# Optimization experiments

Hardware: AMD Instinct MI355X
Metric: run time of the kernel (lower is better)

## Reference

```python
import jax, jax.numpy as jnp
import numpy as np

T, B, E, H = 4096, 2, 1024, 16          # seq, batch, embed, heads
W = 256                                  # one-sided attention window (attention_window=512 // 2)
G = 64                                   # number of global tokens (first G positions)
D = E // H
NEG = -1e9


def _band_mask():
    # valid key position for band slot j at query t is t - W + j in [0, T)
    pos = jnp.arange(T)[:, None] - W + jnp.arange(2 * W + 1)[None, :]
    return (pos >= 0) & (pos < T)  # [T, 2W+1]


def _chunk_blocks(x):
    # x: [b, t, h, d] -> key/value blocks [b, nc, 3w, h, d]; block c covers positions [c*w - w, c*w + 2w)
    b, t, h, d = x.shape
    nc = t // W
    xp = jnp.pad(x, ((0, 0), (W, 2 * W), (0, 0), (0, 0)))
    idx = jnp.arange(nc)[:, None] * W + jnp.arange(3 * W)[None, :]
    return xp[:, idx]


def _band_qk(q, k):
    # q,k: [b,t,h,d] -> banded scores [b,t,h,2w+1] (Longformer sliding_chunks_matmul_qk)
    b, t, h, d = q.shape
    nc = t // W
    qc = q.reshape(b, nc, W, h, d)
    kb = _chunk_blocks(k)
    scores = jnp.einsum('bcxhd,bcyhd->bhcxy', qc, kb)          # y in [0, 3w)
    y_idx = jnp.arange(W)[:, None] + jnp.arange(2 * W + 1)[None, :]  # [w, 2w+1]
    band = jnp.take_along_axis(scores, y_idx[None, None, None], axis=-1)
    band = band.reshape(b, h, t, 2 * W + 1).transpose(0, 2, 1, 3)
    return jnp.where(_band_mask()[None, :, None, :], band, NEG)


def _band_pv(p, v):
    # p: [b,t,h,2w+1], v: [b,t,h,d] -> [b,t,h,d] (sliding_chunks_matmul_pv)
    b, t, h, _ = p.shape
    nc = t // W
    pb = p.transpose(0, 2, 1, 3).reshape(b, h, nc, W, 2 * W + 1)
    x = jnp.arange(W)
    y_idx = x[:, None] + jnp.arange(2 * W + 1)[None, :]
    p3 = jnp.zeros((b, h, nc, W, 3 * W), p.dtype).at[:, :, :, x[:, None], y_idx].set(pb)
    vb = _chunk_blocks(v)
    out = jnp.einsum('bhcxy,bcyhd->bcxhd', p3, vb)
    return out.reshape(b, t, h, -1)


def setup_inputs() -> dict:
    key = jax.random.key(0)
    ks = jax.random.split(key, 16)
    s = 0.02
    inp = {
        'query': jax.random.normal(ks[0], (T, B, E), jnp.float32),
        'attn_mask': jnp.concatenate([jnp.ones((B, G), jnp.int64), jnp.zeros((B, T - G), jnp.int64)], axis=1),
        'Wq': jax.random.normal(ks[1], (E, E), jnp.float32) * s, 'bq': jnp.zeros((E,), jnp.float32),
        'Wk': jax.random.normal(ks[2], (E, E), jnp.float32) * s, 'bk': jnp.zeros((E,), jnp.float32),
        'Wv': jax.random.normal(ks[3], (E, E), jnp.float32) * s, 'bv': jnp.zeros((E,), jnp.float32),
        'Wqg': jax.random.normal(ks[4], (E, E), jnp.float32) * s, 'bqg': jnp.zeros((E,), jnp.float32),
        'Wkg': jax.random.normal(ks[5], (E, E), jnp.float32) * s, 'bkg': jnp.zeros((E,), jnp.float32),
        'Wvg': jax.random.normal(ks[6], (E, E), jnp.float32) * s, 'bvg': jnp.zeros((E,), jnp.float32),
        'Wo': jax.random.normal(ks[7], (E, E), jnp.float32) * s, 'bo': jnp.zeros((E,), jnp.float32),
    }
    return inp


def reference(query, attn_mask, Wq, bq, Wk, bk, Wv, bv, Wqg, bqg, Wkg, bkg, Wvg, bvg, Wo, bo):
    del attn_mask  # structure fixed: first G tokens are global, no padding
    scaling = D ** -0.5
    x = query.transpose(1, 0, 2)                      # [b, t, e]
    q = ((x @ Wq.T + bq) * scaling).reshape(B, T, H, D)
    k = (x @ Wk.T + bk).reshape(B, T, H, D)
    v = (x @ Wv.T + bv).reshape(B, T, H, D)

    band = _band_qk(q, k)                             # [b,t,h,2w+1]
    sel_w = jnp.einsum('blhd,bshd->blhs', q, k[:, :G])  # every token attends global keys
    aw = jnp.concatenate([sel_w, band], axis=-1)
    probs = jax.nn.softmax(aw.astype(jnp.float32), axis=-1).astype(aw.dtype)

    attn = jnp.einsum('blhs,bshd->blhd', probs[..., :G], v[:, :G])
    attn = attn + _band_pv(probs[..., G:], v)         # [b,t,h,d]

    # global tokens attend everything with the *_global projections
    qg = ((x[:, :G] @ Wqg.T + bqg) * scaling).reshape(B, G, H, D)
    kg = (x @ Wkg.T + bkg).reshape(B, T, H, D)
    vg = (x @ Wvg.T + bvg).reshape(B, T, H, D)
    gs = jnp.einsum('bghd,bthd->bhgt', qg, kg)
    gp = jax.nn.softmax(gs.astype(jnp.float32), axis=-1).astype(gs.dtype)
    gout = jnp.einsum('bhgt,bthd->bghd', gp, vg)
    attn = attn.at[:, :G].set(gout)

    out = attn.reshape(B, T, E).transpose(1, 0, 2) @ Wo.T + bo  # [t, b, e]
    return out
```

## Files before the change

kernel.cpp:

```cpp
#include <hip/hip_runtime.h>
#include <hip/hip_bf16.h>

typedef unsigned short u16;
typedef __bf16 bf16x8 __attribute__((ext_vector_type(8)));
typedef float  f32x4  __attribute__((ext_vector_type(4)));

constexpr int TT = 4096;
constexpr int BBATCH = 2;
constexpr int EE = 1024;
constexpr int HH = 16;
constexpr int DD = 64;
constexpr int WQ = 256;
constexpr int GG = 64;
constexpr int NSPLIT = 8;

__device__ __forceinline__ u16 f2bf(float f) {
    union { float f; unsigned int i; } c; c.f = f;
    unsigned int x = c.i;
    return (u16)((x + 0x7fffu + ((x >> 16) & 1u)) >> 16);
}
__device__ __forceinline__ unsigned cvt_pk_bf16(float a, float b) {
    unsigned r;
    asm("v_cvt_pk_bf16_f32 %0, %1, %2" : "=v"(r) : "v"(a), "v"(b));
    return r;
}
__device__ __forceinline__ uint4 pack8(float4 a, float4 b) {
    uint4 r;
    r.x = (unsigned)f2bf(a.x) | ((unsigned)f2bf(a.y) << 16);
    r.y = (unsigned)f2bf(a.z) | ((unsigned)f2bf(a.w) << 16);
    r.z = (unsigned)f2bf(b.x) | ((unsigned)f2bf(b.y) << 16);
    r.w = (unsigned)f2bf(b.z) | ((unsigned)f2bf(b.w) << 16);
    return r;
}

__device__ __forceinline__ void g2l16(const u16* g, u16* l) {
    __builtin_amdgcn_global_load_lds(
        (const __attribute__((address_space(1))) void*)g,
        (__attribute__((address_space(3))) void*)l, 16, 0, 0);
}

__device__ __forceinline__ void xcd_swizzle(int& bx, int& by) {
    bx = blockIdx.x; by = blockIdx.y;
    if ((gridDim.y & 7) == 0) {
        const int g   = blockIdx.x + blockIdx.y * gridDim.x;
        const int idx = g >> 3;
        bx = idx % gridDim.x;
        by = (g & 7) + ((idx / gridDim.x) << 3);
    }
}

struct WPtrs { const float* p[7]; };
__global__ __launch_bounds__(256) void conv_kernel(
    WPtrs wp, const float* __restrict__ query, u16* __restrict__ wb, u16* __restrict__ xb)
{
    const size_t i8 = ((size_t)blockIdx.x * 256 + threadIdx.x) << 3;
    const size_t WTOT = (size_t)7 << 20;
    const float* src;
    u16* dst;
    if (i8 < WTOT) {
        const int which = (int)(i8 >> 20);
        src = wp.p[which] + (i8 & (((size_t)1 << 20) - 1));
        dst = wb + i8;
    } else {
        const size_t j = i8 - WTOT;
        const size_t e = j & (EE - 1);
        const size_t t = (j >> 10) & (TT - 1);
        const size_t b = j >> 22;
        src = query + (t * BBATCH + b) * EE + e;
        dst = xb + j;
    }
    const float4 f0 = *(const float4*)src;
    const float4 f1 = *(const float4*)(src + 4);
    *(uint4*)dst = pack8(f0, f1);
}

template<int C_F32, int PERMA_QG, int PERMC_TB>
__global__ __launch_bounds__(256) void gemm_kernel(
    const u16* __restrict__ A, const u16* __restrict__ W, const float* __restrict__ bias,
    void* __restrict__ Cv, float scale)
{
    const int tid = threadIdx.x, lane = tid & 63, w = tid >> 6;
    const int wm = w >> 1, wn = w & 1;
    int bx, by;
    xcd_swizzle(bx, by);
    const int m0 = by << 7, n0 = bx << 7;

    __shared__ __align__(16) u16 As[2 * 128 * 32];
    __shared__ __align__(16) u16 Bs[2 * 128 * 32];

    const int lrow = lane >> 2;
    const int lcol = (lane & 3) << 3;
    auto arow = [](int m) -> size_t {
        return PERMA_QG ? (size_t)(((m >> 6) << 12) | (m & 63)) : (size_t)m;
    };
    const u16* gA0 = A + arow(m0 + (w << 4) + lrow) * EE + lcol;
    const u16* gA1 = A + arow(m0 + 64 + (w << 4) + lrow) * EE + lcol;
    const u16* gB0 = W + (size_t)(n0 + (w << 4) + lrow) * EE + lcol;
    const u16* gB1 = gB0 + (size_t)64 * EE;
    u16* lA0 = As + (w << 9);
    u16* lA1 = As + 2048 + (w << 9);
    u16* lB0 = Bs + (w << 9);
    u16* lB1 = Bs + 2048 + (w << 9);

    f32x4 acc[4][4];
#pragma unroll
    for (int i = 0; i < 4; i++)
#pragma unroll
        for (int j = 0; j < 4; j++)
            acc[i][j] = (f32x4){0.f, 0.f, 0.f, 0.f};

    const int fr = lane & 15;
    const int fq = (lane >> 4) << 3;

    for (int k0 = 0; k0 < EE; k0 += 64) {
        g2l16(gA0 + k0, lA0);  g2l16(gA0 + k0 + 32, lA0 + 4096);
        g2l16(gA1 + k0, lA1);  g2l16(gA1 + k0 + 32, lA1 + 4096);
        g2l16(gB0 + k0, lB0);  g2l16(gB0 + k0 + 32, lB0 + 4096);
        g2l16(gB1 + k0, lB1);  g2l16(gB1 + k0 + 32, lB1 + 4096);
        __syncthreads();
#pragma unroll
        for (int p = 0; p < 2; p++) {
            bf16x8 af[4], bfv[4];
#pragma unroll
            for (int i = 0; i < 4; i++)
                af[i] = *(const bf16x8*)&As[p * 4096 + ((wm << 6) + (i << 4) + fr) * 32 + fq];
#pragma unroll
            for (int j = 0; j < 4; j++)
                bfv[j] = *(const bf16x8*)&Bs[p * 4096 + ((wn << 6) + (j << 4) + fr) * 32 + fq];
#pragma unroll
            for (int i = 0; i < 4; i++)
#pragma unroll
                for (int j = 0; j < 4; j++)
                    acc[i][j] = __builtin_amdgcn_mfma_f32_16x16x32_bf16(af[i], bfv[j], acc[i][j], 0, 0, 0);
        }
        __syncthreads();
    }

    const int colbase = n0 + (wn << 6);
    const int rowbase = m0 + (wm << 6) + ((lane >> 4) << 2);
#pragma unroll
    for (int j = 0; j < 4; j++) {
        const int col = colbase + (j << 4) + fr;
        const float bv = bias[col];
#pragma unroll
        for (int i = 0; i < 4; i++) {
#pragma unroll
            for (int r = 0; r < 4; r++) {
                const int row = rowbase + (i << 4) + r;
                const float val = (acc[i][j][r] + bv) * scale;
                const size_t dst = (size_t)(PERMC_TB ? (((row & (TT - 1)) << 1) | (row >> 12)) : row) * EE + col;
                if (C_F32) ((float*)Cv)[dst] = val;
                else       ((u16*)Cv)[dst]   = f2bf(val);
            }
        }
    }
}

struct FusedArgs { u16* out[3]; const float* bias[3]; float scale[3]; int vseg; };

template<int NSEG, int CF32, int PERMC>
__global__ __launch_bounds__(256, 2) void gemm_pipe_kernel(
    const u16* __restrict__ A, const u16* __restrict__ W, FusedArgs fa)
{
    const int tid = threadIdx.x, lane = tid & 63, w = tid >> 6;
    const int wm = w >> 1, wn = w & 1;
    int bx, by;
    xcd_swizzle(bx, by);
    const int m0 = by << 7, n0 = bx << 7;

    __shared__ __align__(16) u16 As[2][8192];
    __shared__ __align__(16) u16 Bs[2][8192];

    const int srow = lane >> 3;
    const int scol = ((lane & 7) ^ srow) << 3;
    const u16* gA = A + (size_t)(m0 + (w << 5) + srow) * EE + scol;
    const u16* gB = W + (size_t)(n0 + (w << 5) + srow) * EE + scol;
    u16* lA = &As[0][0] + (w << 11);
    u16* lB = &Bs[0][0] + (w << 11);

    f32x4 acc[4][4];
#pragma unroll
    for (int i = 0; i < 4; i++)
#pragma unroll
        for (int j = 0; j < 4; j++)
            acc[i][j] = (f32x4){0.f, 0.f, 0.f, 0.f};

    const int fr = lane & 15;
    const int qb = (lane >> 4) << 4;
    const int xr = (fr & 7) << 4;

    auto stageA = [&](int k0, int buf) {
#pragma unroll
        for (int l = 0; l < 4; l++)
            g2l16(gA + (size_t)(l << 3) * EE + k0, lA + buf * 8192 + (l << 9));
    };
    auto stageB = [&](int k0, int buf) {
#pragma unroll
        for (int l = 0; l < 4; l++)
            g2l16(gB + (size_t)(l << 3) * EE + k0, lB + buf * 8192 + (l << 9));
    };

    stageA(0, 0);
    stageB(0, 0);
    __syncthreads();

    constexpr int NT = EE / 64;
#pragma unroll 2
    for (int t = 0; t < NT; t++) {
        const int buf = t & 1;
        const bool pf = (t + 1 < NT);
        const int kn = (t + 1) << 6;
        bf16x8 af[4], bfv[4];

#pragma unroll
        for (int mi = 0; mi < 4; mi++)
            af[mi] = *(const bf16x8*)((const char*)&As[buf][0] +
                      ((((wm << 6) + (mi << 4) + fr)) << 7) + (qb ^ xr));
#pragma unroll
        for (int nj = 0; nj < 4; nj++)
            bfv[nj] = *(const bf16x8*)((const char*)&Bs[buf][0] +
                      ((((wn << 6) + (nj << 4) + fr)) << 7) + (qb ^ xr));
        if (pf) stageA(kn, buf ^ 1);
        __builtin_amdgcn_s_barrier();
        __builtin_amdgcn_s_setprio(1);
#pragma unroll
        for (int mi = 0; mi < 4; mi++)
#pragma unroll
            for (int nj = 0; nj < 4; nj++)
                acc[mi][nj] = __builtin_amdgcn_mfma_f32_16x16x32_bf16(af[mi], bfv[nj], acc[mi][nj], 0, 0, 0);
        __builtin_amdgcn_s_setprio(0);
        __builtin_amdgcn_s_barrier();

#pragma unroll
        for (int mi = 0; mi < 4; mi++)
            af[mi] = *(const bf16x8*)((const char*)&As[buf][0] +
                      ((((wm << 6) + (mi << 4) + fr)) << 7) + ((64 | qb) ^ xr));
#pragma unroll
        for (int nj = 0; nj < 4; nj++)
            bfv[nj] = *(const bf16x8*)((const char*)&Bs[buf][0] +
                      ((((wn << 6) + (nj << 4) + fr)) << 7) + ((64 | qb) ^ xr));
        if (pf) stageB(kn, buf ^ 1);
        __builtin_amdgcn_s_barrier();
        __builtin_amdgcn_s_setprio(1);
#pragma unroll
        for (int mi = 0; mi < 4; mi++)
#pragma unroll
            for (int nj = 0; nj < 4; nj++)
                acc[mi][nj] = __builtin_amdgcn_mfma_f32_16x16x32_bf16(af[mi], bfv[nj], acc[mi][nj], 0, 0, 0);
        __builtin_amdgcn_s_setprio(0);
        __syncthreads();
    }

    const int seg = (NSEG > 1) ? (n0 >> 10) : 0;
    u16* outp = fa.out[seg];
    const float* bp = fa.bias[seg];
    const float scl = fa.scale[seg];
    const bool vtr = (NSEG > 1) && (seg == fa.vseg);

    const int colbase = n0 + (wn << 6);
    const int rowbase = m0 + (wm << 6) + ((lane >> 4) << 2);
#pragma unroll
    for (int j = 0; j < 4; j++) {
        const int col = colbase + (j << 4) + fr;
        const int cl  = col & (EE - 1);
        const float bv = bp[cl];
#pragma unroll
        for (int i = 0; i < 4; i++) {
            if (vtr) {
                const int row0 = rowbase + (i << 4);
                const int bb = row0 >> 12, t = row0 & (TT - 1);
                const int hh = cl >> 6, d = cl & 63;
                ushort4 pk;
                pk.x = f2bf((acc[i][j][0] + bv) * scl);
                pk.y = f2bf((acc[i][j][1] + bv) * scl);
                pk.z = f2bf((acc[i][j][2] + bv) * scl);
                pk.w = f2bf((acc[i][j][3] + bv) * scl);
                *(ushort4*)(outp + (((size_t)(bb * HH + hh) * DD + d) * TT + t)) = pk;
            } else {
#pragma unroll
                for (int r = 0; r < 4; r++) {
                    const int row = rowbase + (i << 4) + r;
                    const float val = (acc[i][j][r] + bv) * scl;
                    const size_t drow = PERMC ? (size_t)(((row & (TT - 1)) << 1) | (row >> 12))
                                              : (size_t)row;
                    if (CF32) ((float*)outp)[drow * EE + cl] = val;
                    else      outp[drow * EE + cl] = f2bf(val);
                }
            }
        }
    }
}

__global__ __launch_bounds__(256) void band_attn_kernel(
    const u16* __restrict__ q, const u16* __restrict__ k, const u16* __restrict__ vt,
    u16* __restrict__ attnb)
{
    const int tid  = threadIdx.x;
    const int lane = tid & 63;
    const int w    = tid >> 6;
    const int col  = lane & 15;
    const int quad = lane >> 4;

    const int qt = blockIdx.x >> 5;
    const int bh = blockIdx.x & 31;
    const int h  = bh & (HH - 1);
    const int b  = bh >> 4;
    const int t0 = qt << 6;

    __shared__ __align__(16) u16 Ks[2][64][72];
    __shared__ __align__(16) u16 Vs[2][64][72];
    __shared__ __align__(16) u16 Ps[4][16][72];

    const size_t base   = (size_t)b * TT * EE + (size_t)h * DD;
    const size_t vtbase = (size_t)bh * DD * TT;

    const u16* qp = q + base + (size_t)(t0 + (w << 4) + col) * EE + (quad << 3);
    const bf16x8 qf0 = *(const bf16x8*)qp;
    const bf16x8 qf1 = *(const bf16x8*)(qp + 32);

    float m_i = -1e30f, l_i = 0.f;
    f32x4 acc_o[4];
#pragma unroll
    for (int nt = 0; nt < 4; nt++) acc_o[nt] = (f32x4){0.f, 0.f, 0.f, 0.f};

    const int c_lo = 1 + ((t0 < WQ) ? ((WQ - t0) >> 6) : 0);
    const int c_hi = min(9, 1 + ((TT + WQ - 64 - t0) >> 6));
    const int NTL  = 2 + c_hi - c_lo;

    const int srow  = tid >> 2;
    const int spart = (tid & 3) << 4;

    uint4 kr0, kr1, vr0, vr1;
    auto issue_loads = [&](int i) {
        const int kpos0 = (i == 0) ? 0 : (t0 - WQ + ((c_lo + i - 2) << 6));
        const u16* ks = k + base + (size_t)(kpos0 + srow) * EE + spart;
        const u16* vs = vt + vtbase + (size_t)srow * TT + kpos0 + spart;
        kr0 = *(const uint4*)ks;
        kr1 = *(const uint4*)(ks + 8);
        vr0 = *(const uint4*)vs;
        vr1 = *(const uint4*)(vs + 8);
    };
    auto write_stage = [&](int buf) {
        *(uint4*)&Ks[buf][srow][spart]     = kr0;
        *(uint4*)&Ks[buf][srow][spart + 8] = kr1;
        *(uint4*)&Vs[buf][srow][spart]     = vr0;
        *(uint4*)&Vs[buf][srow][spart + 8] = vr1;
    };

    issue_loads(0);
    write_stage(0);
    int buf = 0;

    const int qrow = (w << 4) + col;
    const int alsrc0 = (lane & 48) | ((lane >> 2) & 12);

#pragma unroll 1
    for (int i = 0; i < NTL; i++) {
        __syncthreads();
        const int c     = c_lo + i - 1;
        const int jbase = (i > 0 && (c == 1 || c == 9)) ? ((c - 1) << 6) : -1;
        const bool pf   = (i + 1 < NTL);
        if (pf) issue_loads(i + 1);

        f32x4 sT[4];
#pragma unroll
        for (int nt = 0; nt < 4; nt++) {
            const bf16x8 kf0 = *(const bf16x8*)&Ks[buf][(nt << 4) + col][quad << 3];
            const bf16x8 kf1 = *(const bf16x8*)&Ks[buf][(nt << 4) + col][32 + (quad << 3)];
            f32x4 s = (f32x4){0.f, 0.f, 0.f, 0.f};
            s = __builtin_amdgcn_mfma_f32_16x16x32_bf16(kf0, qf0, s, 0, 0, 0);
            s = __builtin_amdgcn_mfma_f32_16x16x32_bf16(kf1, qf1, s, 0, 0, 0);
            sT[nt] = s;
        }

        if (jbase >= 0) {
#pragma unroll
            for (int nt = 0; nt < 4; nt++) {
#pragma unroll
                for (int r = 0; r < 4; r++) {
                    const int jp = jbase + (nt << 4) + (quad << 2) + r;
                    const bool ok = (jp >= qrow) && (jp <= qrow + 2 * WQ);
                    if (!ok) sT[nt][r] = -1e30f;
                }
            }
        }

        float mx = sT[0][0];
#pragma unroll
        for (int nt = 0; nt < 4; nt++)
#pragma unroll
            for (int r = 0; r < 4; r++) mx = fmaxf(mx, sT[nt][r]);
        mx = fmaxf(mx, __shfl_xor(mx, 16));
        mx = fmaxf(mx, __shfl_xor(mx, 32));
        const float m_new = fmaxf(m_i, mx);
        const float alpha = __expf(m_i - m_new);
        m_i = m_new;
        l_i *= alpha;
        float ps = 0.f;
#pragma unroll
        for (int nt = 0; nt < 4; nt++)
#pragma unroll
            for (int r = 0; r < 4; r++) {
                const float e = __expf(sT[nt][r] - m_new);
                sT[nt][r] = e;
                ps += e;
            }
        ps += __shfl_xor(ps, 16);
        ps += __shfl_xor(ps, 32);
        l_i += ps;

        float al[4];
#pragma unroll
        for (int r = 0; r < 4; r++) al[r] = __shfl(alpha, alsrc0 | r);
#pragma unroll
        for (int nt = 0; nt < 4; nt++)
#pragma unroll
            for (int r = 0; r < 4; r++) acc_o[nt][r] *= al[r];

#pragma unroll
        for (int nt = 0; nt < 4; nt++) {
            uint2 pk2;
            pk2.x = cvt_pk_bf16(sT[nt][0], sT[nt][1]);
            pk2.y = cvt_pk_bf16(sT[nt][2], sT[nt][3]);
            *(uint2*)&Ps[w][col][(nt << 4) + (quad << 2)] = pk2;
        }

        const bf16x8 pf0 = *(const bf16x8*)&Ps[w][col][quad << 3];
        const bf16x8 pf1 = *(const bf16x8*)&Ps[w][col][32 + (quad << 3)];

#pragma unroll
        for (int nt = 0; nt < 4; nt++) {
            const bf16x8 vf0 = *(const bf16x8*)&Vs[buf][(nt << 4) + col][quad << 3];
            const bf16x8 vf1 = *(const bf16x8*)&Vs[buf][(nt << 4) + col][32 + (quad << 3)];
            acc_o[nt] = __builtin_amdgcn_mfma_f32_16x16x32_bf16(pf0, vf0, acc_o[nt], 0, 0, 0);
            acc_o[nt] = __builtin_amdgcn_mfma_f32_16x16x32_bf16(pf1, vf1, acc_o[nt], 0, 0, 0);
        }

        if (pf) write_stage(buf ^ 1);
        buf ^= 1;
    }

    float inv[4];
#pragma unroll
    for (int r = 0; r < 4; r++) inv[r] = 1.f / __shfl(l_i, alsrc0 | r);
#pragma unroll
    for (int nt = 0; nt < 4; nt++) {
#pragma unroll
        for (int r = 0; r < 4; r++) {
            const int t = t0 + (w << 4) + (quad << 2) + r;
            attnb[base + (size_t)t * EE + (nt << 4) + col] = f2bf(acc_o[nt][r] * inv[r]);
        }
    }
}

__global__ __launch_bounds__(256) void global_attn_flash_kernel(
    const u16* __restrict__ qg, const u16* __restrict__ kg, const u16* __restrict__ vgt,
    float* __restrict__ Op, float* __restrict__ Ml, float* __restrict__ Ll)
{
    const int tid  = threadIdx.x;
    const int lane = tid & 63;
    const int w    = tid >> 6;
    const int col  = lane & 15;
    const int quad = lane >> 4;

    const int s  = blockIdx.x & (NSPLIT - 1);
    const int h  = (blockIdx.x >> 3) & (HH - 1);
    const int b  = blockIdx.x >> 7;
    const int k0pos = s * (TT / NSPLIT);

    __shared__ __align__(16) u16 Ks[2][64][72];
    __shared__ __align__(16) u16 Vs[2][64][72];
    __shared__ __align__(16) u16 Ps[4][16][72];

    const size_t base   = (size_t)b * TT * EE + (size_t)h * DD;
    const size_t vtbase = (size_t)((b << 4) | h) * DD * TT;

    const u16* qp = qg + (size_t)(b * GG + (w << 4) + col) * EE + (size_t)h * DD + (quad << 3);
    const bf16x8 qf0 = *(const bf16x8*)qp;
    const bf16x8 qf1 = *(const bf16x8*)(qp + 32);

    float m_i = -1e30f, l_i = 0.f;
    f32x4 acc_o[4];
#pragma unroll
    for (int nt = 0; nt < 4; nt++) acc_o[nt] = (f32x4){0.f, 0.f, 0.f, 0.f};

    constexpr int NTL = TT / NSPLIT / 64;
    const int srow  = tid >> 2;
    const int spart = (tid & 3) << 4;

    uint4 kr0, kr1, vr0, vr1;
    auto issue_loads = [&](int i) {
        const int kpos0 = k0pos + (i << 6);
        const u16* ks = kg + base + (size_t)(kpos0 + srow) * EE + spart;
        const u16* vs = vgt + vtbase + (size_t)srow * TT + kpos0 + spart;
        kr0 = *(const uint4*)ks;
        kr1 = *(const uint4*)(ks + 8);
        vr0 = *(const uint4*)vs;
        vr1 = *(const uint4*)(vs + 8);
    };
    auto write_stage = [&](int buf) {
        *(uint4*)&Ks[buf][srow][spart]     = kr0;
        *(uint4*)&Ks[buf][srow][spart + 8] = kr1;
        *(uint4*)&Vs[buf][srow][spart]     = vr0;
        *(uint4*)&Vs[buf][srow][spart + 8] = vr1;
    };

    issue_loads(0);
    write_stage(0);
    int buf = 0;

    const int alsrc0 = (lane & 48) | ((lane >> 2) & 12);

#pragma unroll 1
    for (int i = 0; i < NTL; i++) {
        __syncthreads();
        const bool pf = (i + 1 < NTL);
        if (pf) issue_loads(i + 1);

        f32x4 sT[4];
#pragma unroll
        for (int nt = 0; nt < 4; nt++) {
            const bf16x8 kf0 = *(const bf16x8*)&Ks[buf][(nt << 4) + col][quad << 3];
            const bf16x8 kf1 = *(const bf16x8*)&Ks[buf][(nt << 4) + col][32 + (quad << 3)];
            f32x4 sv = (f32x4){0.f, 0.f, 0.f, 0.f};
            sv = __builtin_amdgcn_mfma_f32_16x16x32_bf16(kf0, qf0, sv, 0, 0, 0);
            sv = __builtin_amdgcn_mfma_f32_16x16x32_bf16(kf1, qf1, sv, 0, 0, 0);
            sT[nt] = sv;
        }

        float mx = sT[0][0];
#pragma unroll
        for (int nt = 0; nt < 4; nt++)
#pragma unroll
            for (int r = 0; r < 4; r++) mx = fmaxf(mx, sT[nt][r]);
        mx = fmaxf(mx, __shfl_xor(mx, 16));
        mx = fmaxf(mx, __shfl_xor(mx, 32));
        const float m_new = fmaxf(m_i, mx);
        const float alpha = __expf(m_i - m_new);
        m_i = m_new;
        l_i *= alpha;
        float ps = 0.f;
#pragma unroll
        for (int nt = 0; nt < 4; nt++)
#pragma unroll
            for (int r = 0; r < 4; r++) {
                const float e = __expf(sT[nt][r] - m_new);
                sT[nt][r] = e;
                ps += e;
            }
        ps += __shfl_xor(ps, 16);
        ps += __shfl_xor(ps, 32);
        l_i += ps;

        float al[4];
#pragma unroll
        for (int r = 0; r < 4; r++) al[r] = __shfl(alpha, alsrc0 | r);
#pragma unroll
        for (int nt = 0; nt < 4; nt++)
#pragma unroll
            for (int r = 0; r < 4; r++) acc_o[nt][r] *= al[r];

#pragma unroll
        for (int nt = 0; nt < 4; nt++) {
            uint2 pk2;
            pk2.x = cvt_pk_bf16(sT[nt][0], sT[nt][1]);
            pk2.y = cvt_pk_bf16(sT[nt][2], sT[nt][3]);
            *(uint2*)&Ps[w][col][(nt << 4) + (quad << 2)] = pk2;
        }

        const bf16x8 pf0 = *(const bf16x8*)&Ps[w][col][quad << 3];
        const bf16x8 pf1 = *(const bf16x8*)&Ps[w][col][32 + (quad << 3)];

#pragma unroll
        for (int nt = 0; nt < 4; nt++) {
            const bf16x8 vf0 = *(const bf16x8*)&Vs[buf][(nt << 4) + col][quad << 3];
            const bf16x8 vf1 = *(const bf16x8*)&Vs[buf][(nt << 4) + col][32 + (quad << 3)];
            acc_o[nt] = __builtin_amdgcn_mfma_f32_16x16x32_bf16(pf0, vf0, acc_o[nt], 0, 0, 0);
            acc_o[nt] = __builtin_amdgcn_mfma_f32_16x16x32_bf16(pf1, vf1, acc_o[nt], 0, 0, 0);
        }

        if (pf) write_stage(buf ^ 1);
        buf ^= 1;
    }

    const size_t obase = (size_t)blockIdx.x * GG * DD;
#pragma unroll
    for (int nt = 0; nt < 4; nt++) {
#pragma unroll
        for (int r = 0; r < 4; r++) {
            const int row = (w << 4) + (quad << 2) + r;
            Op[obase + (size_t)row * DD + (nt << 4) + col] = acc_o[nt][r];
        }
    }
    if (quad == 0) {
        Ml[blockIdx.x * GG + (w << 4) + col] = m_i;
        Ll[blockIdx.x * GG + (w << 4) + col] = l_i;
    }
}

__global__ __launch_bounds__(256) void global_combine_kernel(
    const float* __restrict__ Op, const float* __restrict__ Ml, const float* __restrict__ Ll,
    u16* __restrict__ attnb)
{
    const int bh  = blockIdx.x;
    const int b   = bh >> 4;
    const int h   = bh & (HH - 1);
    const int row = threadIdx.x >> 2;
    const int d0  = (threadIdx.x & 3) << 4;

    float mv[NSPLIT];
    float m = -1e30f;
#pragma unroll
    for (int s = 0; s < NSPLIT; s++) {
        mv[s] = Ml[(bh * NSPLIT + s) * GG + row];
        m = fmaxf(m, mv[s]);
    }
    float l = 0.f;
    float sc[NSPLIT];
#pragma unroll
    for (int s = 0; s < NSPLIT; s++) {
        sc[s] = __expf(mv[s] - m);
        l += Ll[(bh * NSPLIT + s) * GG + row] * sc[s];
    }
    float o[16];
#pragma unroll
    for (int j = 0; j < 16; j++) o[j] = 0.f;
#pragma unroll
    for (int s = 0; s < NSPLIT; s++) {
        const float* src = Op + ((size_t)(bh * NSPLIT + s) * GG + row) * DD + d0;
        const float f = sc[s];
#pragma unroll
        for (int j = 0; j < 16; j += 4) {
            const float4 v4 = *(const float4*)(src + j);
            o[j + 0] = fmaf(v4.x, f, o[j + 0]);
            o[j + 1] = fmaf(v4.y, f, o[j + 1]);
            o[j + 2] = fmaf(v4.z, f, o[j + 2]);
            o[j + 3] = fmaf(v4.w, f, o[j + 3]);
        }
    }
    const float inv = 1.f / l;
    u16* dst = attnb + ((size_t)b * TT + row) * EE + (size_t)h * DD + d0;
#pragma unroll
    for (int j = 0; j < 16; j++) dst[j] = f2bf(o[j] * inv);
}

extern "C" void kernel_launch(void* const* d_in, const int* in_sizes, int n_in,
                              void* d_out, int out_size, void* d_ws, size_t ws_size,
                              hipStream_t stream)
{
    (void)in_sizes; (void)n_in; (void)out_size; (void)ws_size;
    const float* query = (const float*)d_in[0];
    const float* Wq  = (const float*)d_in[2];  const float* bq  = (const float*)d_in[3];
    const float* Wk  = (const float*)d_in[4];  const float* bk  = (const float*)d_in[5];
    const float* Wv  = (const float*)d_in[6];  const float* bv  = (const float*)d_in[7];
    const float* Wqg = (const float*)d_in[8];  const float* bqg = (const float*)d_in[9];
    const float* Wkg = (const float*)d_in[10]; const float* bkg = (const float*)d_in[11];
    const float* Wvg = (const float*)d_in[12]; const float* bvg = (const float*)d_in[13];
    const float* Wo  = (const float*)d_in[14]; const float* bo  = (const float*)d_in[15];

    const size_t nfull = (size_t)BBATCH * TT * EE;
    const size_t wsz   = (size_t)1 << 20;
    u16* xb    = (u16*)d_ws;
    u16* wb    = xb + nfull;
    u16* slotA = wb + 7 * wsz;
    u16* slotB = slotA + nfull;
    u16* slotC = slotB + nfull;
    u16* qg    = slotC + nfull;
    float* Op  = (float*)(qg + (size_t)BBATCH * GG * EE);
    float* Ml  = Op + (size_t)BBATCH * HH * NSPLIT * GG * DD;
    float* Ll  = Ml + (size_t)BBATCH * HH * NSPLIT * GG;
    u16* attnb = xb;

    WPtrs wp;
    wp.p[0] = Wq; wp.p[1] = Wk; wp.p[2] = Wv;
    wp.p[3] = Wkg; wp.p[4] = Wvg; wp.p[5] = Wqg; wp.p[6] = Wo;

    const dim3 blk(256);
    const dim3 gF2(16, 64);
    const dim3 gF3(24, 64);
    const dim3 gFull(8, 64);
    const dim3 gQg(8, 1);
    const float sc = 0.125f;

    conv_kernel<<<7680, blk, 0, stream>>>(wp, query, wb, xb);

    gemm_kernel<0, 1, 0><<<gQg, blk, 0, stream>>>(xb, wb + 5 * wsz, bqg, qg, sc);

    FusedArgs fa2;
    fa2.out[0] = slotA; fa2.out[1] = slotB; fa2.out[2] = nullptr;
    fa2.bias[0] = bkg;  fa2.bias[1] = bvg;  fa2.bias[2] = nullptr;
    fa2.scale[0] = 1.f; fa2.scale[1] = 1.f; fa2.scale[2] = 1.f;
    fa2.vseg = 1;
    gemm_pipe_kernel<2, 0, 0><<<gF2, blk, 0, stream>>>(xb, wb + 3 * wsz, fa2);
    global_attn_flash_kernel<<<BBATCH * HH * NSPLIT, blk, 0, stream>>>(qg, slotA, slotB, Op, Ml, Ll);

    FusedArgs fa3;
    fa3.out[0] = slotA; fa3.out[1] = slotB; fa3.out[2] = slotC;
    fa3.bias[0] = bq;   fa3.bias[1] = bk;   fa3.bias[2] = bv;
    fa3.scale[0] = sc;  fa3.scale[1] = 1.f; fa3.scale[2] = 1.f;
    fa3.vseg = 2;
    gemm_pipe_kernel<3, 0, 0><<<gF3, blk, 0, stream>>>(xb, wb, fa3);

    band_attn_kernel<<<BBATCH * HH * (TT / 64), blk, 0, stream>>>(slotA, slotB, slotC, attnb);
    global_combine_kernel<<<BBATCH * HH, blk, 0, stream>>>(Op, Ml, Ll, attnb);

    FusedArgs faO;
    faO.out[0] = (u16*)d_out; faO.out[1] = nullptr; faO.out[2] = nullptr;
    faO.bias[0] = bo;         faO.bias[1] = nullptr; faO.bias[2] = nullptr;
    faO.scale[0] = 1.f;       faO.scale[1] = 1.f;    faO.scale[2] = 1.f;
    faO.vseg = -1;
    gemm_pipe_kernel<1, 1, 1><<<gFull, blk, 0, stream>>>(attnb, wb + 6 * wsz, faO);
}
```

Baseline: 341.4 us.

## Use single-buffered GEMM and lazy softmax rescaling in attention kernels

Replaces the double-buffered, barrier-interleaved GEMM main loop with a simpler single-buffered loop: load a K tile, sync, compute two k-halves, sync. This halves LDS use and drops the min-blocks launch bound, which could raise occupancy, but global loads no longer overlap with MFMA work. Separately, both flash-attention kernels now skip the running-max update and accumulator rescale unless some lane's new max exceeds the old one by more than 8. That saves exps and multiplies but lets exponentials reach up to e^8 before renormalising.

Result: slower. 352.4 us (+3.2%).

```diff
diff --git a/kernel.cpp b/kernel.cpp
--- a/kernel.cpp
+++ b/kernel.cpp
@@ -159,7 +159,7 @@
 struct FusedArgs { u16* out[3]; const float* bias[3]; float scale[3]; int vseg; };
 
 template<int NSEG, int CF32, int PERMC>
-__global__ __launch_bounds__(256, 2) void gemm_pipe_kernel(
+__global__ __launch_bounds__(256) void gemm_sb_kernel(
     const u16* __restrict__ A, const u16* __restrict__ W, FusedArgs fa)
 {
     const int tid = threadIdx.x, lane = tid & 63, w = tid >> 6;
@@ -168,15 +168,15 @@
     xcd_swizzle(bx, by);
     const int m0 = by << 7, n0 = bx << 7;
 
-    __shared__ __align__(16) u16 As[2][8192];
-    __shared__ __align__(16) u16 Bs[2][8192];
+    __shared__ __align__(16) u16 As[8192];
+    __shared__ __align__(16) u16 Bs[8192];
 
     const int srow = lane >> 3;
     const int scol = ((lane & 7) ^ srow) << 3;
     const u16* gA = A + (size_t)(m0 + (w << 5) + srow) * EE + scol;
     const u16* gB = W + (size_t)(n0 + (w << 5) + srow) * EE + scol;
-    u16* lA = &As[0][0] + (w << 11);
-    u16* lB = &Bs[0][0] + (w << 11);
+    u16* lA = As + (w << 11);
+    u16* lB = Bs + (w << 11);
 
     f32x4 acc[4][4];
 #pragma unroll
@@ -189,65 +189,31 @@
     const int qb = (lane >> 4) << 4;
     const int xr = (fr & 7) << 4;
 
-    auto stageA = [&](int k0, int buf) {
-#pragma unroll
-        for (int l = 0; l < 4; l++)
-            g2l16(gA + (size_t)(l << 3) * EE + k0, lA + buf * 8192 + (l << 9));
-    };
-    auto stageB = [&](int k0, int buf) {
-#pragma unroll
-        for (int l = 0; l < 4; l++)
-            g2l16(gB + (size_t)(l << 3) * EE + k0, lB + buf * 8192 + (l << 9));
-    };
-
-    stageA(0, 0);
-    stageB(0, 0);
-    __syncthreads();
-
-    constexpr int NT = EE / 64;
-#pragma unroll 2
-    for (int t = 0; t < NT; t++) {
-        const int buf = t & 1;
-        const bool pf = (t + 1 < NT);
-        const int kn = (t + 1) << 6;
-        bf16x8 af[4], bfv[4];
-
-#pragma unroll
-        for (int mi = 0; mi < 4; mi++)
-            af[mi] = *(const bf16x8*)((const char*)&As[buf][0] +
-                      ((((wm << 6) + (mi << 4) + fr)) << 7) + (qb ^ xr));
-#pragma unroll
-        for (int nj = 0; nj < 4; nj++)
-            bfv[nj] = *(const bf16x8*)((const char*)&Bs[buf][0] +
-                      ((((wn << 6) + (nj << 4) + fr)) << 7) + (qb ^ xr));
-        if (pf) stageA(kn, buf ^ 1);
-        __builtin_amdgcn_s_barrier();
-        __builtin_amdgcn_s_setprio(1);
-#pragma unroll
-        for (int mi = 0; mi < 4; mi++)
+    for (int t = 0; t < EE / 64; t++) {
+        const int k0 = t << 6;
+#pragma unroll
+        for (int l = 0; l < 4; l++) {
+            g2l16(gA + (size_t)(l << 3) * EE + k0, lA + (l << 9));
+            g2l16(gB + (size_t)(l << 3) * EE + k0, lB + (l << 9));
+        }
+        __syncthreads();
+#pragma unroll
+        for (int kh = 0; kh < 2; kh++) {
+            bf16x8 af[4], bfv[4];
+#pragma unroll
+            for (int mi = 0; mi < 4; mi++)
+                af[mi] = *(const bf16x8*)((const char*)As +
+                          ((((wm << 6) + (mi << 4) + fr)) << 7) + (((kh << 6) | qb) ^ xr));
 #pragma unroll
             for (int nj = 0; nj < 4; nj++)
-                acc[mi][nj] = __builtin_amdgcn_mfma_f32_16x16x32_bf16(af[mi], bfv[nj], acc[mi][nj], 0, 0, 0);
-        __builtin_amdgcn_s_setprio(0);
-        __builtin_amdgcn_s_barrier();
-
-#pragma unroll
-        for (int mi = 0; mi < 4; mi++)
-            af[mi] = *(const bf16x8*)((const char*)&As[buf][0] +
-                      ((((wm << 6) + (mi << 4) + fr)) << 7) + ((64 | qb) ^ xr));
-#pragma unroll
-        for (int nj = 0; nj < 4; nj++)
-            bfv[nj] = *(const bf16x8*)((const char*)&Bs[buf][0] +
-                      ((((wn << 6) + (nj << 4) + fr)) << 7) + ((64 | qb) ^ xr));
-        if (pf) stageB(kn, buf ^ 1);
-        __builtin_amdgcn_s_barrier();
-        __builtin_amdgcn_s_setprio(1);
-#pragma unroll
-        for (int mi = 0; mi < 4; mi++)
-#pragma unroll
-            for (int nj = 0; nj < 4; nj++)
-                acc[mi][nj] = __builtin_amdgcn_mfma_f32_16x16x32_bf16(af[mi], bfv[nj], acc[mi][nj], 0, 0, 0);
-        __builtin_amdgcn_s_setprio(0);
+                bfv[nj] = *(const bf16x8*)((const char*)Bs +
+                          ((((wn << 6) + (nj << 4) + fr)) << 7) + (((kh << 6) | qb) ^ xr));
+#pragma unroll
+            for (int mi = 0; mi < 4; mi++)
+#pragma unroll
+                for (int nj = 0; nj < 4; nj++)
+                    acc[mi][nj] = __builtin_amdgcn_mfma_f32_16x16x32_bf16(af[mi], bfv[nj], acc[mi][nj], 0, 0, 0);
+        }
         __syncthreads();
     }
 
@@ -392,30 +358,33 @@
             for (int r = 0; r < 4; r++) mx = fmaxf(mx, sT[nt][r]);
         mx = fmaxf(mx, __shfl_xor(mx, 16));
         mx = fmaxf(mx, __shfl_xor(mx, 32));
-        const float m_new = fmaxf(m_i, mx);
-        const float alpha = __expf(m_i - m_new);
-        m_i = m_new;
-        l_i *= alpha;
+
+        if (!__all(mx - m_i <= 8.0f)) {
+            const float m_new = fmaxf(m_i, mx);
+            const float alpha = __expf(m_i - m_new);
+            m_i = m_new;
+            l_i *= alpha;
+            float al[4];
+#pragma unroll
+            for (int r = 0; r < 4; r++) al[r] = __shfl(alpha, alsrc0 | r);
+#pragma unroll
+            for (int nt = 0; nt < 4; nt++)
+#pragma unroll
+                for (int r = 0; r < 4; r++) acc_o[nt][r] *= al[r];
+        }
+
         float ps = 0.f;
 #pragma unroll
         for (int nt = 0; nt < 4; nt++)
 #pragma unroll
             for (int r = 0; r < 4; r++) {
-                const float e = __expf(sT[nt][r] - m_new);
+                const float e = __expf(sT[nt][r] - m_i);
                 sT[nt][r] = e;
                 ps += e;
             }
         ps += __shfl_xor(ps, 16);
         ps += __shfl_xor(ps, 32);
         l_i += ps;
-
-        float al[4];
-#pragma unroll
-        for (int r = 0; r < 4; r++) al[r] = __shfl(alpha, alsrc0 | r);
-#pragma unroll
-        for (int nt = 0; nt < 4; nt++)
-#pragma unroll
-            for (int r = 0; r < 4; r++) acc_o[nt][r] *= al[r];
 
 #pragma unroll
         for (int nt = 0; nt < 4; nt++) {
@@ -535,30 +504,33 @@
             for (int r = 0; r < 4; r++) mx = fmaxf(mx, sT[nt][r]);
         mx = fmaxf(mx, __shfl_xor(mx, 16));
         mx = fmaxf(mx, __shfl_xor(mx, 32));
-        const float m_new = fmaxf(m_i, mx);
-        const float alpha = __expf(m_i - m_new);
-        m_i = m_new;
-        l_i *= alpha;
+
+        if (!__all(mx - m_i <= 8.0f)) {
+            const float m_new = fmaxf(m_i, mx);
+            const float alpha = __expf(m_i - m_new);
+            m_i = m_new;
+            l_i *= alpha;
+            float al[4];
+#pragma unroll
+            for (int r = 0; r < 4; r++) al[r] = __shfl(alpha, alsrc0 | r);
+#pragma unroll
+            for (int nt = 0; nt < 4; nt++)
+#pragma unroll
+                for (int r = 0; r < 4; r++) acc_o[nt][r] *= al[r];
+        }
+
         float ps = 0.f;
 #pragma unroll
         for (int nt = 0; nt < 4; nt++)
 #pragma unroll
             for (int r = 0; r < 4; r++) {
-                const float e = __expf(sT[nt][r] - m_new);
+                const float e = __expf(sT[nt][r] - m_i);
                 sT[nt][r] = e;
                 ps += e;
             }
         ps += __shfl_xor(ps, 16);
         ps += __shfl_xor(ps, 32);
         l_i += ps;
-
-        float al[4];
-#pragma unroll
-        for (int r = 0; r < 4; r++) al[r] = __shfl(alpha, alsrc0 | r);
-#pragma unroll
-        for (int nt = 0; nt < 4; nt++)
-#pragma unroll
-            for (int r = 0; r < 4; r++) acc_o[nt][r] *= al[r];
 
 #pragma unroll
         for (int nt = 0; nt < 4; nt++) {
@@ -691,7 +663,7 @@
     fa2.bias[0] = bkg;  fa2.bias[1] = bvg;  fa2.bias[2] = nullptr;
     fa2.scale[0] = 1.f; fa2.scale[1] = 1.f; fa2.scale[2] = 1.f;
     fa2.vseg = 1;
-    gemm_pipe_kernel<2, 0, 0><<<gF2, blk, 0, stream>>>(xb, wb + 3 * wsz, fa2);
+    gemm_sb_kernel<2, 0, 0><<<gF2, blk, 0, stream>>>(xb, wb + 3 * wsz, fa2);
     global_attn_flash_kernel<<<BBATCH * HH * NSPLIT, blk, 0, stream>>>(qg, slotA, slotB, Op, Ml, Ll);
 
     FusedArgs fa3;
@@ -699,7 +671,7 @@
     fa3.bias[0] = bq;   fa3.bias[1] = bk;   fa3.bias[2] = bv;
     fa3.scale[0] = sc;  fa3.scale[1] = 1.f; fa3.scale[2] = 1.f;
     fa3.vseg = 2;
-    gemm_pipe_kernel<3, 0, 0><<<gF3, blk, 0, stream>>>(xb, wb, fa3);
+    gemm_sb_kernel<3, 0, 0><<<gF3, blk, 0, stream>>>(xb, wb, fa3);
 
     band_attn_kernel<<<BBATCH * HH * (TT / 64), blk, 0, stream>>>(slotA, slotB, slotC, attnb);
     global_combine_kernel<<<BBATCH * HH, blk, 0, stream>>>(Op, Ml, Ll, attnb);
@@ -709,5 +681,5 @@
     faO.bias[0] = bo;         faO.bias[1] = nullptr; faO.bias[2] = nullptr;
     faO.scale[0] = 1.f;       faO.scale[1] = 1.f;    faO.scale[2] = 1.f;
     faO.vseg = -1;
-    gemm_pipe_kernel<1, 1, 1><<<gFull, blk, 0, stream>>>(attnb, wb + 6 * wsz, faO);
-}
+    gemm_sb_kernel<1, 1, 1><<<gFull, blk, 0, stream>>>(attnb, wb + 6 * wsz, faO);
+}
```
